# Kernel tuning notes

Hardware: AMD Instinct MI355X
Metric: run time of the kernel (lower is better)

## Reference

```python
import jax, jax.numpy as jnp
import numpy as np

B, N, M, D, H = 8, 2048, 2048, 512, 8


def setup_inputs() -> dict:
    key = jax.random.key(0)
    ks = jax.random.split(key, 12)
    std = D ** (-0.5)
    inp = {
        "k": jax.random.normal(ks[0], (B, N, D), jnp.float32),
        "v": jax.random.normal(ks[1], (B, N, D), jnp.float32),
        "q": jax.random.normal(ks[2], (B, M, D), jnp.float32),
        # per-head projections, stacked over the head axis: [H, D, D]
        "Wk": jax.random.normal(ks[3], (H, D, D), jnp.float32) * std,
        "bk": jax.random.normal(ks[4], (H, D), jnp.float32) * 0.01,
        "Wv": jax.random.normal(ks[5], (H, D, D), jnp.float32) * std,
        "bv": jax.random.normal(ks[6], (H, D), jnp.float32) * 0.01,
        "Wq": jax.random.normal(ks[7], (H, D, D), jnp.float32) * std,
        "bq": jax.random.normal(ks[8], (H, D), jnp.float32) * 0.01,
        # final linear: input ordering is (hidden_dim, head) flattened -> H*D
        "Wo": jax.random.normal(ks[9], (H * D, D), jnp.float32) * (H * D) ** (-0.5),
        "bo": jax.random.normal(ks[10], (D,), jnp.float32) * 0.01,
    }
    return inp


def reference(k, v, q, Wk, bk, Wv, bv, Wq, bq, Wo, bo):
    # Per-head linear projections (torch loops over heads; here batched over h).
    # nn.Linear computes x @ W.T + b; Wk here stores W.T directly as [H, D, D].
    k_ = jnp.einsum("bnd,hde->bhne", k, Wk) + bk[None, :, None, :]  # [B,H,N,D]
    v_ = jnp.einsum("bnd,hde->bhne", v, Wv) + bv[None, :, None, :]  # [B,H,N,D]
    q_ = jnp.einsum("bmd,hde->bhme", q, Wq) + bq[None, :, None, :]  # [B,H,M,D]

    scale = D ** 0.5
    scores = jnp.einsum("bhmd,bhnd->bhmn", q_, k_) / scale  # [B,H,M,N]
    weights = jax.nn.softmax(scores, axis=-1)
    out = jnp.einsum("bhmn,bhnd->bhmd", weights, v_)  # [B,H,M,D]

    # torch: stack(outs, dim=-1) -> [B,M,D,H], then view -> [B,M,D*H]
    outs = jnp.transpose(out, (0, 2, 3, 1)).reshape(B, M, D * H)
    # matching flatten order (d-major, h-minor) requires Wo rows ordered d*H+h;
    # setup generates Wo random so any consistent ordering is faithful.
    rep = outs @ Wo + bo  # [B,M,D]
    return rep
```

## Files before the change

### kernel.cpp

```cpp
#include <hip/hip_runtime.h>
#include <hip/hip_bf16.h>
#include <cstdint>
#include <cstddef>

typedef __bf16 bf16x8 __attribute__((ext_vector_type(8)));
typedef __bf16 bf16x4 __attribute__((ext_vector_type(4)));
typedef float floatx4 __attribute__((ext_vector_type(4)));

#define MFMA16(a, b, c) __builtin_amdgcn_mfma_f32_16x16x32_bf16((a), (b), (c), 0, 0, 0)

__device__ __forceinline__ void load_lds16(const __bf16* g, __bf16* l) {
  __builtin_amdgcn_global_load_lds(
      (const __attribute__((address_space(1))) uint32_t*)(g),
      (__attribute__((address_space(3))) uint32_t*)(l), 16, 0, 0);
}

__global__ __launch_bounds__(256) void tw_t(const float* __restrict__ W,
                                            __bf16* __restrict__ Wt, float scale) {
  __shared__ float tile[64][65];
  int h = blockIdx.z, d0 = blockIdx.y * 64, e0 = blockIdx.x * 64;
  int tx = threadIdx.x & 15, ty = threadIdx.x >> 4;
  const float* src = W + ((size_t)h * 512 + d0) * 512 + e0;
#pragma unroll
  for (int j = 0; j < 4; ++j) {
    int dd = ty + j * 16;
    float4 f = *(const float4*)&src[(size_t)dd * 512 + tx * 4];
    tile[dd][tx * 4 + 0] = f.x; tile[dd][tx * 4 + 1] = f.y;
    tile[dd][tx * 4 + 2] = f.z; tile[dd][tx * 4 + 3] = f.w;
  }
  __syncthreads();
  __bf16* dst = Wt + ((size_t)h * 512 + e0) * 512 + d0;
#pragma unroll
  for (int j = 0; j < 4; ++j) {
    int ee = ty + j * 16;
    bf16x4 v;
#pragma unroll
    for (int x = 0; x < 4; ++x) v[x] = (__bf16)(tile[tx * 4 + x][ee] * scale);
    *(bf16x4*)&dst[(size_t)ee * 512 + tx * 4] = v;
  }
}

__global__ __launch_bounds__(256) void wo_t(const float* __restrict__ Wo,
                                            __bf16* __restrict__ Wot) {
  __shared__ float tile[64][65];
  int h = blockIdx.z, d0 = blockIdx.y * 64, e0 = blockIdx.x * 64;
  int tx = threadIdx.x & 15, ty = threadIdx.x >> 4;
#pragma unroll
  for (int j = 0; j < 4; ++j) {
    int dd = ty + j * 16;
    float4 f = *(const float4*)&Wo[(size_t)((d0 + dd) * 8 + h) * 512 + e0 + tx * 4];
    tile[dd][tx * 4 + 0] = f.x; tile[dd][tx * 4 + 1] = f.y;
    tile[dd][tx * 4 + 2] = f.z; tile[dd][tx * 4 + 3] = f.w;
  }
  __syncthreads();
#pragma unroll
  for (int j = 0; j < 4; ++j) {
    int ee = ty + j * 16;
    bf16x4 v;
#pragma unroll
    for (int x = 0; x < 4; ++x) v[x] = (__bf16)tile[tx * 4 + x][ee];
    *(bf16x4*)&Wot[(size_t)(e0 + ee) * 4096 + h * 512 + d0 + tx * 4] = v;
  }
}

template <int EPI, bool AF32>
__global__ __launch_bounds__(256) void gemm_bt(const void* __restrict__ Ap,
                                               const __bf16* __restrict__ Bt,
                                               const float* __restrict__ bias,
                                               void* __restrict__ Cout,
                                               int N, int K, float bscale) {
  __shared__ __align__(16) __bf16 sA[128][72];
  __shared__ __align__(16) __bf16 sB[128][72];
  const int tid = threadIdx.x;
  const int lane = tid & 63;
  const int wave = tid >> 6;
  const int lr = lane & 15;
  const int lq = lane >> 4;
  const int wm = (wave >> 1) * 64;
  const int wn = (wave & 1) * 64;
  const int bx = blockIdx.x, by = blockIdx.y;
  const int srow = tid >> 3;
  const int scol = (tid & 7) << 3;

  const floatx4 z4 = {0.f, 0.f, 0.f, 0.f};
  floatx4 acc[4][4];
#pragma unroll
  for (int i = 0; i < 4; ++i)
#pragma unroll
    for (int j = 0; j < 4; ++j) acc[i][j] = z4;

  const size_t abase = (size_t)(by * 128) * K;
  const size_t bbase = (size_t)(bx * 128) * K;

  for (int k0 = 0; k0 < K; k0 += 64) {
#pragma unroll
    for (int p = 0; p < 4; ++p) {
      int row = p * 32 + srow;
      if (AF32) {
        const float* A = (const float*)Ap;
        float4 f0 = *(const float4*)&A[abase + (size_t)row * K + k0 + scol];
        float4 f1 = *(const float4*)&A[abase + (size_t)row * K + k0 + scol + 4];
        bf16x8 v;
        v[0] = (__bf16)f0.x; v[1] = (__bf16)f0.y; v[2] = (__bf16)f0.z; v[3] = (__bf16)f0.w;
        v[4] = (__bf16)f1.x; v[5] = (__bf16)f1.y; v[6] = (__bf16)f1.z; v[7] = (__bf16)f1.w;
        *(bf16x8*)&sA[row][scol] = v;
      } else {
        const __bf16* A = (const __bf16*)Ap;
        *(bf16x8*)&sA[row][scol] = *(const bf16x8*)&A[abase + (size_t)row * K + k0 + scol];
      }
      *(bf16x8*)&sB[row][scol] = *(const bf16x8*)&Bt[bbase + (size_t)row * K + k0 + scol];
    }
    __syncthreads();
#pragma unroll
    for (int ks = 0; ks < 2; ++ks) {
      bf16x8 af[4], bfr[4];
#pragma unroll
      for (int mt = 0; mt < 4; ++mt)
        af[mt] = *(const bf16x8*)&sA[wm + mt * 16 + lr][ks * 32 + lq * 8];
#pragma unroll
      for (int nt = 0; nt < 4; ++nt)
        bfr[nt] = *(const bf16x8*)&sB[wn + nt * 16 + lr][ks * 32 + lq * 8];
#pragma unroll
      for (int mt = 0; mt < 4; ++mt)
#pragma unroll
        for (int nt = 0; nt < 4; ++nt) acc[mt][nt] = MFMA16(af[mt], bfr[nt], acc[mt][nt]);
    }
    __syncthreads();
  }

#pragma unroll
  for (int mt = 0; mt < 4; ++mt) {
#pragma unroll
    for (int nt = 0; nt < 4; ++nt) {
      int col = bx * 128 + wn + nt * 16 + lr;
      int row0 = by * 128 + wm + mt * 16 + lq * 4;
      float bcol = bias[col] * bscale;
      if (EPI == 0) {
        __bf16* dst = (__bf16*)Cout;
        int h = col >> 9, e = col & 511;
#pragma unroll
        for (int r = 0; r < 4; ++r) {
          int row = row0 + r;
          int b = row >> 11, m = row & 2047;
          dst[((size_t)((b << 3) | h) * 2048 + m) * 512 + e] = (__bf16)(acc[mt][nt][r] + bcol);
        }
      } else if (EPI == 1) {
        __bf16* dst = (__bf16*)Cout;
        int h = col >> 9, e = col & 511;
        int b = row0 >> 11, n = row0 & 2047;
        bf16x4 pk;
#pragma unroll
        for (int r = 0; r < 4; ++r) pk[r] = (__bf16)(acc[mt][nt][r] + bcol);
        *(bf16x4*)&dst[((size_t)((b << 3) | h) * 512 + e) * 2048 + n] = pk;
      } else {
        float* dst = (float*)Cout;
#pragma unroll
        for (int r = 0; r < 4; ++r) {
          int row = row0 + r;
          dst[(size_t)row * N + col] = acc[mt][nt][r] + bcol;
        }
      }
    }
  }
}

__global__ __launch_bounds__(512, 2) void attn_kernel(const __bf16* __restrict__ Qp,
                                                      const __bf16* __restrict__ Kp,
                                                      const __bf16* __restrict__ Vt,
                                                      __bf16* __restrict__ Outs) {
  __shared__ __align__(16) __bf16 kls[2][32 * 512];
  __shared__ __align__(16) __bf16 vls[2][512 * 32];
  __shared__ __align__(16) __bf16 pls[8][16 * 40];
  const int tid = threadIdx.x;
  const int lane = tid & 63;
  const int wave = tid >> 6;
  const int lr = lane & 15;
  const int lq = lane >> 4;
  const int blk = blockIdx.x;
  const int bh = blk >> 4;
  const int mblk = blk & 15;
  const int m0 = mblk * 128 + wave * 16;
  const __bf16* Qb = Qp + (size_t)bh * (2048 * 512);
  const __bf16* Kb = Kp + (size_t)bh * (2048 * 512);
  const __bf16* Vb = Vt + (size_t)bh * (512 * 2048);

  int gK[4], gV[4];
#pragma unroll
  for (int i = 0; i < 4; ++i) {
    int q = i * 512 + tid;
    int rK = q >> 6;
    gK[i] = rK * 512 + ((q & 63) ^ (rK & 7)) * 8;
    int eV = q >> 2;
    gV[i] = eV * 2048 + ((q & 3) ^ (eV & 3)) * 8;
  }

  bf16x8 qf[16];
#pragma unroll
  for (int ks = 0; ks < 16; ++ks)
    qf[ks] = *(const bf16x8*)&Qb[(size_t)(m0 + lr) * 512 + ks * 32 + lq * 8];

  const floatx4 z4 = {0.f, 0.f, 0.f, 0.f};
  floatx4 o[32];
#pragma unroll
  for (int et = 0; et < 32; ++et) o[et] = z4;
  float lsum[4] = {0.f, 0.f, 0.f, 0.f};

#pragma unroll
  for (int i = 0; i < 4; ++i) {
    load_lds16(Kb + gK[i], &kls[0][i * 4096 + wave * 512]);
    load_lds16(Vb + gV[i], &vls[0][i * 4096 + wave * 512]);
  }
  __syncthreads();

  for (int t = 0; t < 64; ++t) {
    const int cur = t & 1;
    if (t < 63) {
      const __bf16* kg = Kb + (size_t)(t + 1) * (32 * 512);
      const __bf16* vg = Vb + (t + 1) * 32;
#pragma unroll
      for (int i = 0; i < 4; ++i) {
        load_lds16(kg + gK[i], &kls[cur ^ 1][i * 4096 + wave * 512]);
        load_lds16(vg + gV[i], &vls[cur ^ 1][i * 4096 + wave * 512]);
      }
    }
    floatx4 s0 = z4, s1 = z4;
    const __bf16* kc = kls[cur];
#pragma unroll
    for (int ks = 0; ks < 16; ++ks) {
      int cidx = ((ks * 4 + lq) ^ (lr & 7)) * 8;
      bf16x8 k0 = *(const bf16x8*)&kc[lr * 512 + cidx];
      bf16x8 k1 = *(const bf16x8*)&kc[(16 + lr) * 512 + cidx];
      s0 = MFMA16(qf[ks], k0, s0);
      s1 = MFMA16(qf[ks], k1, s1);
    }
#pragma unroll
    for (int r = 0; r < 4; ++r) {
      float p0 = __expf(s0[r]);
      float p1 = __expf(s1[r]);
      lsum[r] += p0 + p1;
      pls[wave][(lq * 4 + r) * 40 + lr] = (__bf16)p0;
      pls[wave][(lq * 4 + r) * 40 + 16 + lr] = (__bf16)p1;
    }
    bf16x8 pf = *(const bf16x8*)&pls[wave][lr * 40 + lq * 8];
    const __bf16* vc = vls[cur];
#pragma unroll
    for (int et = 0; et < 32; ++et) {
      int e = et * 16 + lr;
      bf16x8 vf = *(const bf16x8*)&vc[e * 32 + ((lq ^ (e & 3)) * 8)];
      o[et] = MFMA16(pf, vf, o[et]);
    }
    __syncthreads();
  }

  float inv[4];
#pragma unroll
  for (int r = 0; r < 4; ++r) {
    float t = lsum[r];
    t += __shfl_xor(t, 1);
    t += __shfl_xor(t, 2);
    t += __shfl_xor(t, 4);
    t += __shfl_xor(t, 8);
    inv[r] = 1.0f / t;
  }
  int b = bh >> 3, h = bh & 7;
  size_t rowbase = ((size_t)b * 2048 + m0 + lq * 4) * 4096 + h * 512;
#pragma unroll
  for (int et = 0; et < 32; ++et)
#pragma unroll
    for (int r = 0; r < 4; ++r)
      Outs[rowbase + (size_t)r * 4096 + et * 16 + lr] = (__bf16)(o[et][r] * inv[r]);
}

extern "C" void kernel_launch(void* const* d_in, const int* in_sizes, int n_in,
                              void* d_out, int out_size, void* d_ws, size_t ws_size,
                              hipStream_t stream) {
  (void)in_sizes; (void)n_in; (void)out_size;
  const float* kin = (const float*)d_in[0];
  const float* vin = (const float*)d_in[1];
  const float* qin = (const float*)d_in[2];
  const float* Wk  = (const float*)d_in[3];
  const float* bk  = (const float*)d_in[4];
  const float* Wv  = (const float*)d_in[5];
  const float* bv  = (const float*)d_in[6];
  const float* Wq  = (const float*)d_in[7];
  const float* bq  = (const float*)d_in[8];
  const float* Wo  = (const float*)d_in[9];
  const float* bo  = (const float*)d_in[10];
  float* out = (float*)d_out;
  char* ws = (char*)d_ws;

  const float scale = 0.044194173824159216f;

  const size_t SZ_W = (size_t)4096 * 512 * 2;
  const size_t SZ_B = (size_t)8 * 2048 * 512 * 2;
  const size_t FIXED = 4 * SZ_W;

  int nb = 1;
  if (ws_size >= FIXED + 8 * 4 * SZ_B) nb = 8;
  else if (ws_size >= FIXED + 4 * 4 * SZ_B) nb = 4;
  else if (ws_size >= FIXED + 2 * 4 * SZ_B) nb = 2;

  __bf16* Wkt = (__bf16*)(ws);
  __bf16* Wvt = (__bf16*)(ws + SZ_W);
  __bf16* Wqt = (__bf16*)(ws + 2 * SZ_W);
  __bf16* Wot = (__bf16*)(ws + 3 * SZ_W);
  char* chunkbase = ws + FIXED;
  __bf16* kproj = (__bf16*)(chunkbase);
  __bf16* qproj = (__bf16*)(chunkbase + (size_t)nb * SZ_B);
  __bf16* vt    = (__bf16*)(chunkbase + (size_t)nb * 2 * SZ_B);
  __bf16* outs  = (__bf16*)(chunkbase + (size_t)nb * 3 * SZ_B);

  tw_t<<<dim3(8, 8, 8), dim3(256), 0, stream>>>(Wk, Wkt, 1.0f);
  tw_t<<<dim3(8, 8, 8), dim3(256), 0, stream>>>(Wv, Wvt, 1.0f);
  tw_t<<<dim3(8, 8, 8), dim3(256), 0, stream>>>(Wq, Wqt, scale);
  wo_t<<<dim3(8, 8, 8), dim3(256), 0, stream>>>(Wo, Wot);

  for (int b0 = 0; b0 < 8; b0 += nb) {
    const float* kc = kin + (size_t)b0 * 2048 * 512;
    const float* vc = vin + (size_t)b0 * 2048 * 512;
    const float* qc = qin + (size_t)b0 * 2048 * 512;
    gemm_bt<0, true><<<dim3(32, nb * 16), dim3(256), 0, stream>>>(kc, Wkt, bk, (void*)kproj, 4096, 512, 1.0f);
    gemm_bt<0, true><<<dim3(32, nb * 16), dim3(256), 0, stream>>>(qc, Wqt, bq, (void*)qproj, 4096, 512, scale);
    gemm_bt<1, true><<<dim3(32, nb * 16), dim3(256), 0, stream>>>(vc, Wvt, bv, (void*)vt, 4096, 512, 1.0f);
    attn_kernel<<<dim3(nb * 128), dim3(512), 0, stream>>>(qproj, kproj, vt, outs);
    gemm_bt<2, false><<<dim3(4, nb * 16), dim3(256), 0, stream>>>(
        (void*)outs, Wot, bo, (void*)(out + (size_t)b0 * 2048 * 512), 512, 4096, 1.0f);
  }
}
```

Baseline: 1.767 ms.

## Split PV across waves by output column and software-pipeline PV one tile behind

Each wave previously computed P·V for its own 16 query rows over all 512 output columns, reading the whole V tile from LDS. Now the P tiles of all waves are shared in LDS, and each wave computes all 128 rows for a 64-column slice of V. This cuts redundant V fragment reads from LDS and reuses each V fragment across 8 row tiles. The PV step is also delayed by one iteration, so the V load for tile t overlaps with the QK and exp work. The row sums are reduced through LDS before normalisation. This adds LDS traffic for P and relies on the single barrier per iteration to order the double-buffered P/V accesses.

```diff
diff --git a/kernel.cpp b/kernel.cpp
--- a/kernel.cpp
+++ b/kernel.cpp
@@ -170,7 +170,8 @@
                                                       __bf16* __restrict__ Outs) {
   __shared__ __align__(16) __bf16 kls[2][32 * 512];
   __shared__ __align__(16) __bf16 vls[2][512 * 32];
-  __shared__ __align__(16) __bf16 pls[8][16 * 40];
+  __shared__ __align__(16) __bf16 pls[2][128 * 40];
+  __shared__ __align__(16) float l_red[128];
   const int tid = threadIdx.x;
   const int lane = tid & 63;
   const int wave = tid >> 6;
@@ -179,7 +180,9 @@
   const int blk = blockIdx.x;
   const int bh = blk >> 4;
   const int mblk = blk & 15;
-  const int m0 = mblk * 128 + wave * 16;
+  const int qrow0 = wave * 16;
+  const int m0 = mblk * 128 + qrow0;
+  const int e0 = wave * 64;
   const __bf16* Qb = Qp + (size_t)bh * (2048 * 512);
   const __bf16* Kb = Kp + (size_t)bh * (2048 * 512);
   const __bf16* Vb = Vt + (size_t)bh * (512 * 2048);
@@ -200,28 +203,45 @@
     qf[ks] = *(const bf16x8*)&Qb[(size_t)(m0 + lr) * 512 + ks * 32 + lq * 8];
 
   const floatx4 z4 = {0.f, 0.f, 0.f, 0.f};
-  floatx4 o[32];
-#pragma unroll
-  for (int et = 0; et < 32; ++et) o[et] = z4;
+  floatx4 o[8][4];
+#pragma unroll
+  for (int mt = 0; mt < 8; ++mt)
+#pragma unroll
+    for (int et = 0; et < 4; ++et) o[mt][et] = z4;
   float lsum[4] = {0.f, 0.f, 0.f, 0.f};
 
-#pragma unroll
-  for (int i = 0; i < 4; ++i) {
-    load_lds16(Kb + gK[i], &kls[0][i * 4096 + wave * 512]);
-    load_lds16(Vb + gV[i], &vls[0][i * 4096 + wave * 512]);
-  }
+  auto pv_step = [&](const __bf16* pc, const __bf16* vc) {
+    bf16x8 vf[4];
+#pragma unroll
+    for (int et = 0; et < 4; ++et) {
+      int e = e0 + et * 16 + lr;
+      vf[et] = *(const bf16x8*)&vc[e * 32 + ((lq ^ (e & 3)) * 8)];
+    }
+#pragma unroll
+    for (int mt = 0; mt < 8; ++mt) {
+      bf16x8 pf = *(const bf16x8*)&pc[(mt * 16 + lr) * 40 + lq * 8];
+#pragma unroll
+      for (int et = 0; et < 4; ++et) o[mt][et] = MFMA16(pf, vf[et], o[mt][et]);
+    }
+  };
+
+#pragma unroll
+  for (int i = 0; i < 4; ++i) load_lds16(Kb + gK[i], &kls[0][i * 4096 + wave * 512]);
   __syncthreads();
 
   for (int t = 0; t < 64; ++t) {
     const int cur = t & 1;
     if (t < 63) {
       const __bf16* kg = Kb + (size_t)(t + 1) * (32 * 512);
-      const __bf16* vg = Vb + (t + 1) * 32;
-#pragma unroll
-      for (int i = 0; i < 4; ++i) {
+#pragma unroll
+      for (int i = 0; i < 4; ++i)
         load_lds16(kg + gK[i], &kls[cur ^ 1][i * 4096 + wave * 512]);
-        load_lds16(vg + gV[i], &vls[cur ^ 1][i * 4096 + wave * 512]);
-      }
+    }
+    {
+      const __bf16* vg = Vb + t * 32;
+#pragma unroll
+      for (int i = 0; i < 4; ++i)
+        load_lds16(vg + gV[i], &vls[cur][i * 4096 + wave * 512]);
     }
     floatx4 s0 = z4, s1 = z4;
     const __bf16* kc = kls[cur];
@@ -238,37 +258,41 @@
       float p0 = __expf(s0[r]);
       float p1 = __expf(s1[r]);
       lsum[r] += p0 + p1;
-      pls[wave][(lq * 4 + r) * 40 + lr] = (__bf16)p0;
-      pls[wave][(lq * 4 + r) * 40 + 16 + lr] = (__bf16)p1;
-    }
-    bf16x8 pf = *(const bf16x8*)&pls[wave][lr * 40 + lq * 8];
-    const __bf16* vc = vls[cur];
-#pragma unroll
-    for (int et = 0; et < 32; ++et) {
-      int e = et * 16 + lr;
-      bf16x8 vf = *(const bf16x8*)&vc[e * 32 + ((lq ^ (e & 3)) * 8)];
-      o[et] = MFMA16(pf, vf, o[et]);
-    }
+      pls[cur][(qrow0 + lq * 4 + r) * 40 + lr] = (__bf16)p0;
+      pls[cur][(qrow0 + lq * 4 + r) * 40 + 16 + lr] = (__bf16)p1;
+    }
+    if (t > 0) pv_step(pls[cur ^ 1], vls[cur ^ 1]);
     __syncthreads();
   }
-
-  float inv[4];
+  pv_step(pls[1], vls[1]);
+
 #pragma unroll
   for (int r = 0; r < 4; ++r) {
-    float t = lsum[r];
-    t += __shfl_xor(t, 1);
-    t += __shfl_xor(t, 2);
-    t += __shfl_xor(t, 4);
-    t += __shfl_xor(t, 8);
-    inv[r] = 1.0f / t;
-  }
+    float s = lsum[r];
+    s += __shfl_xor(s, 1);
+    s += __shfl_xor(s, 2);
+    s += __shfl_xor(s, 4);
+    s += __shfl_xor(s, 8);
+    lsum[r] = s;
+  }
+  if (lr == 0) {
+#pragma unroll
+    for (int r = 0; r < 4; ++r) l_red[qrow0 + lq * 4 + r] = lsum[r];
+  }
+  __syncthreads();
+
   int b = bh >> 3, h = bh & 7;
-  size_t rowbase = ((size_t)b * 2048 + m0 + lq * 4) * 4096 + h * 512;
-#pragma unroll
-  for (int et = 0; et < 32; ++et)
-#pragma unroll
-    for (int r = 0; r < 4; ++r)
-      Outs[rowbase + (size_t)r * 4096 + et * 16 + lr] = (__bf16)(o[et][r] * inv[r]);
+#pragma unroll
+  for (int mt = 0; mt < 8; ++mt) {
+    float4 lv = *(const float4*)&l_red[mt * 16 + lq * 4];
+    float invr[4] = {1.0f / lv.x, 1.0f / lv.y, 1.0f / lv.z, 1.0f / lv.w};
+    size_t rowbase = ((size_t)b * 2048 + mblk * 128 + mt * 16 + lq * 4) * 4096 + h * 512 + e0;
+#pragma unroll
+    for (int et = 0; et < 4; ++et)
+#pragma unroll
+      for (int r = 0; r < 4; ++r)
+        Outs[rowbase + (size_t)r * 4096 + et * 16 + lr] = (__bf16)(o[mt][et][r] * invr[r]);
+  }
 }
 
 extern "C" void kernel_launch(void* const* d_in, const int* in_sizes, int n_in,
```

Measured after the change: 1.658 ms. 6.1% less time.
